# Performance work log

Hardware: AMD Instinct MI355X
Metric: run time of the kernel (lower is better)

The kernel has to match this reference:

```python
import jax, jax.numpy as jnp
import numpy as np
from jax import lax

B, T, HID, H, DK, DV, K = 2, 2048, 1024, 16, 64, 64, 4
SCALE = float(DK) ** -0.5
EPS = 1e-5


def setup_inputs() -> dict:
    key = jax.random.key(0)
    ks = jax.random.split(key, 12)
    n = lambda k, sh, s=0.02: (jax.random.normal(k, sh, jnp.float32) * s)
    return {
        "x": jax.random.normal(ks[0], (B, T, HID), jnp.float32),
        "Wq": n(ks[1], (H * DK, HID)),
        "Wk": n(ks[2], (H * DK, HID)),
        "Wv": n(ks[3], (H * DV, HID)),
        "Wa": n(ks[4], (H * DV, HID)), "ba": jnp.zeros((H * DV,), jnp.float32),
        "Wb": n(ks[5], (H, HID)), "bb": jnp.zeros((H,), jnp.float32),
        "Wg": n(ks[6], (H * DV, HID)),
        "Wo": n(ks[7], (HID, H * DV)),
        "qcw": n(ks[8], (H * DK, 1, K), 0.3), "qcb": jnp.zeros((H * DK,), jnp.float32),
        "kcw": n(ks[9], (H * DK, 1, K), 0.3), "kcb": jnp.zeros((H * DK,), jnp.float32),
        "vcw": n(ks[10], (H * DV, 1, K), 0.3), "vcb": jnp.zeros((H * DV,), jnp.float32),
        "ln_w": jnp.ones((DV,), jnp.float32), "ln_b": jnp.zeros((DV,), jnp.float32),
    }


def _causal_dwconv_silu(z, w, b):
    # z: [B,T,C], w: [C,1,K] depthwise. Conv1d(padding=K-1) then slice[:T] == causal left-pad.
    zc = z.transpose(0, 2, 1)  # [B,C,T]
    y = lax.conv_general_dilated(zc, w, (1,), [(K - 1, 0)],
                                 dimension_numbers=("NCH", "OIH", "NCH"),
                                 feature_group_count=zc.shape[1])
    return jax.nn.silu((y + b[None, :, None]).transpose(0, 2, 1))


def reference(x, Wq, Wk, Wv, Wa, ba, Wb, bb, Wg, Wo,
              qcw, qcb, kcw, kcb, vcw, vcb, ln_w, ln_b):
    Bb, Tt, _ = x.shape
    q = _causal_dwconv_silu(x @ Wq.T, qcw, qcb).reshape(Bb, Tt, H, DK)
    k = _causal_dwconv_silu(x @ Wk.T, kcw, kcb).reshape(Bb, Tt, H, DK) * SCALE
    v = _causal_dwconv_silu(x @ Wv.T, vcw, vcb).reshape(Bb, Tt, H, DV)
    a = jax.nn.sigmoid(x @ Wa.T + ba).reshape(Bb, Tt, H, DV)
    beta = jax.nn.sigmoid(x @ Wb.T + bb)  # [B,T,H]

    def step(S, inp):
        qt, kt, vt, at, bt = inp  # qt/kt: [B,H,DK], vt/at: [B,H,DV], bt: [B,H]
        err = jnp.einsum("bhij,bhj->bhi", S, kt) - vt          # S@k - v
        S = at[..., None] * S - bt[..., None, None] * (err[..., None] * kt[:, :, None, :])
        o = jnp.einsum("bhij,bhj->bhi", S, qt)                 # S@q
        return S, o

    xs = tuple(jnp.moveaxis(t, 1, 0) for t in (q, k, v, a, beta))  # time-leading
    S0 = jnp.zeros((Bb, H, DV, DK), x.dtype)
    _, o = lax.scan(step, S0, xs)
    o = jnp.moveaxis(o, 0, 1)  # [B,T,H,DV]

    mu = o.mean(-1, keepdims=True)
    var = ((o - mu) ** 2).mean(-1, keepdims=True)
    o = (o - mu) / jnp.sqrt(var + EPS) * ln_w + ln_b

    g = jax.nn.sigmoid(x @ Wg.T).reshape(Bb, Tt, H, DV)
    o = (o * g).reshape(Bb, Tt, H * DV)
    return o @ Wo.T
```

## Files before the change

kernel.cpp:

```cpp
#include <hip/hip_runtime.h>
#include <hip/hip_bf16.h>
#include <cstdint>


using bf16 = __hip_bfloat16;
typedef __bf16 bf16x8 __attribute__((ext_vector_type(8)));
typedef __bf16 bf16x4v __attribute__((ext_vector_type(4)));
typedef float f32x4 __attribute__((ext_vector_type(4)));
typedef float f32x2 __attribute__((ext_vector_type(2)));
typedef unsigned int u32x4 __attribute__((ext_vector_type(4)));
typedef unsigned int u32x2 __attribute__((ext_vector_type(2)));

__device__ __forceinline__ __bf16 cvt_bf16(float f) {
  __hip_bfloat16 h = (__hip_bfloat16)f;
  return *reinterpret_cast<__bf16*>(&h);
}
__device__ __forceinline__ void async_copy16(const void* g, void* l) {
  __builtin_amdgcn_global_load_lds((const __attribute__((address_space(1))) void*)g,
                                   (__attribute__((address_space(3))) void*)l,
                                   16, 0, 0);
}
__device__ __forceinline__ float bcf(unsigned int u) { return __builtin_bit_cast(float, u); }
template <int CTRL>
__device__ __forceinline__ float dpp_f(float x) {
  int y = __builtin_amdgcn_update_dpp(0, __builtin_bit_cast(int, x), CTRL, 0xF, 0xF, true);
  return __builtin_bit_cast(float, y);
}

__global__ __launch_bounds__(256) void cvt_plane_kernel(
    const float* __restrict__ in, bf16* __restrict__ out)
{
  size_t i = ((size_t)blockIdx.x * 256 + threadIdx.x) * 4;
  float4 f = *(const float4*)(in + i);
  bf16x4v t;
  t[0] = cvt_bf16(f.x); t[1] = cvt_bf16(f.y); t[2] = cvt_bf16(f.z); t[3] = cvt_bf16(f.w);
  *(bf16x4v*)((__bf16*)out + i) = t;
}

template <int MODE, bool A_FP32>
__global__ __launch_bounds__(256) void gemm_bt(
    const void* __restrict__ Av, const float* __restrict__ Bt,
    const float* __restrict__ bias, float* __restrict__ Cf, bf16* __restrict__ Cb,
    int M, int N, int K)
{
  __shared__ __align__(16) __bf16 As[128 * 32];
  __shared__ __align__(16) __bf16 Bs[128 * 32];

  const int tid  = threadIdx.x;
  const int lane = tid & 63;
  const int wave = tid >> 6;
  const int tile_m = blockIdx.y * 128;
  const int tile_n = blockIdx.x * 128;
  const int wm = (wave >> 1) * 64;
  const int wn = (wave & 1) * 64;

  const int srow = lane >> 2;
  const int scol = (lane & 3) * 8;

  f32x4 acc[4][4];
#pragma unroll
  for (int i = 0; i < 4; ++i)
#pragma unroll
    for (int j = 0; j < 4; ++j) acc[i][j] = {0.f, 0.f, 0.f, 0.f};

  for (int k0 = 0; k0 < K; k0 += 32) {
    float4 b0[2], b1[2], a0[2], a1[2];
#pragma unroll
    for (int s = 0; s < 2; ++s) {
      int brow = tile_n + s * 64 + wave * 16 + srow;
      if (brow > N - 1) brow = N - 1;
      const float* bp = Bt + (size_t)brow * K + k0 + scol;
      b0[s] = *(const float4*)bp;
      b1[s] = *(const float4*)(bp + 4);
      if (A_FP32) {
        int arow = tile_m + s * 64 + wave * 16 + srow;
        const float* ap = (const float*)Av + (size_t)arow * K + k0 + scol;
        a0[s] = *(const float4*)ap;
        a1[s] = *(const float4*)(ap + 4);
      }
    }
    __syncthreads();
#pragma unroll
    for (int s = 0; s < 2; ++s) {
      if (!A_FP32) {
        int arow = tile_m + s * 64 + wave * 16 + srow;
        async_copy16((const __bf16*)Av + (size_t)arow * K + k0 + scol,
                     &As[(s * 64 + wave * 16 + srow) * 32 + scol]);
      } else {
        bf16x8 ua;
        ua[0] = cvt_bf16(a0[s].x); ua[1] = cvt_bf16(a0[s].y);
        ua[2] = cvt_bf16(a0[s].z); ua[3] = cvt_bf16(a0[s].w);
        ua[4] = cvt_bf16(a1[s].x); ua[5] = cvt_bf16(a1[s].y);
        ua[6] = cvt_bf16(a1[s].z); ua[7] = cvt_bf16(a1[s].w);
        *(bf16x8*)&As[(s * 64 + wave * 16 + srow) * 32 + scol] = ua;
      }
      bf16x8 u;
      u[0] = cvt_bf16(b0[s].x); u[1] = cvt_bf16(b0[s].y);
      u[2] = cvt_bf16(b0[s].z); u[3] = cvt_bf16(b0[s].w);
      u[4] = cvt_bf16(b1[s].x); u[5] = cvt_bf16(b1[s].y);
      u[6] = cvt_bf16(b1[s].z); u[7] = cvt_bf16(b1[s].w);
      *(bf16x8*)&Bs[(s * 64 + wave * 16 + srow) * 32 + scol] = u;
    }
    __syncthreads();

    bf16x8 af[4], bfr[4];
#pragma unroll
    for (int i = 0; i < 4; ++i)
      af[i] = *(const bf16x8*)&As[(wm + i * 16 + (lane & 15)) * 32 + (lane >> 4) * 8];
#pragma unroll
    for (int j = 0; j < 4; ++j)
      bfr[j] = *(const bf16x8*)&Bs[(wn + j * 16 + (lane & 15)) * 32 + (lane >> 4) * 8];

#pragma unroll
    for (int i = 0; i < 4; ++i)
#pragma unroll
      for (int j = 0; j < 4; ++j)
        acc[i][j] = __builtin_amdgcn_mfma_f32_16x16x32_bf16(af[i], bfr[j], acc[i][j], 0, 0, 0);
  }

#pragma unroll
  for (int i = 0; i < 4; ++i) {
#pragma unroll
    for (int j = 0; j < 4; ++j) {
#pragma unroll
      for (int r = 0; r < 4; ++r) {
        int gm = tile_m + wm + i * 16 + (lane >> 4) * 4 + r;
        int gn = tile_n + wn + j * 16 + (lane & 15);
        if (gn < N) {
          float val = acc[i][j][r];
          if (MODE == 3 || MODE == 5) {
            float bv = bias ? bias[gn] : 0.f;
            val = 1.f / (1.f + __expf(-(val + bv)));
          }
          if (MODE == 4)      Cf[(size_t)gm * N + gn] = val;
          else if (MODE == 5) Cf[(size_t)gn * M + gm] = val;
          else                Cb[(size_t)gm * N + gn] = (bf16)val;
        }
      }
    }
  }
}

__global__ __launch_bounds__(256) void mega_gemm(
    const bf16* __restrict__ Av, const float* __restrict__ Wq,
    const float* __restrict__ Wk, const float* __restrict__ Wv,
    const float* __restrict__ Wa, const float* __restrict__ ba,
    bf16* __restrict__ C4, int M, int K)
{
  __shared__ __align__(16) __bf16 As[128 * 32];
  __shared__ __align__(16) __bf16 Bs[128 * 32];

  const int tid  = threadIdx.x;
  const int lane = tid & 63;
  const int wave = tid >> 6;
  const int tile_m = blockIdx.y * 128;
  const int tile_n = blockIdx.x * 128;
  const int grp = tile_n >> 10;
  const int tnl = tile_n & 1023;
  const float* Bt = (grp == 0) ? Wq : (grp == 1) ? Wk : (grp == 2) ? Wv : Wa;
  const int wm = (wave >> 1) * 64;
  const int wn = (wave & 1) * 64;

  const int srow = lane >> 2;
  const int scol = (lane & 3) * 8;

  f32x4 acc[4][4];
#pragma unroll
  for (int i = 0; i < 4; ++i)
#pragma unroll
    for (int j = 0; j < 4; ++j) acc[i][j] = {0.f, 0.f, 0.f, 0.f};

  for (int k0 = 0; k0 < K; k0 += 32) {
    float4 b0[2], b1[2];
#pragma unroll
    for (int s = 0; s < 2; ++s) {
      int brow = tnl + s * 64 + wave * 16 + srow;
      const float* bp = Bt + (size_t)brow * K + k0 + scol;
      b0[s] = *(const float4*)bp;
      b1[s] = *(const float4*)(bp + 4);
    }
    __syncthreads();
#pragma unroll
    for (int s = 0; s < 2; ++s) {
      int arow = tile_m + s * 64 + wave * 16 + srow;
      async_copy16((const __bf16*)Av + (size_t)arow * K + k0 + scol,
                   &As[(s * 64 + wave * 16 + srow) * 32 + scol]);
      bf16x8 u;
      u[0] = cvt_bf16(b0[s].x); u[1] = cvt_bf16(b0[s].y);
      u[2] = cvt_bf16(b0[s].z); u[3] = cvt_bf16(b0[s].w);
      u[4] = cvt_bf16(b1[s].x); u[5] = cvt_bf16(b1[s].y);
      u[6] = cvt_bf16(b1[s].z); u[7] = cvt_bf16(b1[s].w);
      *(bf16x8*)&Bs[(s * 64 + wave * 16 + srow) * 32 + scol] = u;
    }
    __syncthreads();

    bf16x8 af[4], bfr[4];
#pragma unroll
    for (int i = 0; i < 4; ++i)
      af[i] = *(const bf16x8*)&As[(wm + i * 16 + (lane & 15)) * 32 + (lane >> 4) * 8];
#pragma unroll
    for (int j = 0; j < 4; ++j)
      bfr[j] = *(const bf16x8*)&Bs[(wn + j * 16 + (lane & 15)) * 32 + (lane >> 4) * 8];

#pragma unroll
    for (int i = 0; i < 4; ++i)
#pragma unroll
      for (int j = 0; j < 4; ++j)
        acc[i][j] = __builtin_amdgcn_mfma_f32_16x16x32_bf16(af[i], bfr[j], acc[i][j], 0, 0, 0);
  }

  bf16* Cp = (bf16*)((__bf16*)C4 + (size_t)grp * M * 1024);
#pragma unroll
  for (int i = 0; i < 4; ++i) {
#pragma unroll
    for (int j = 0; j < 4; ++j) {
#pragma unroll
      for (int r = 0; r < 4; ++r) {
        int gm = tile_m + wm + i * 16 + (lane >> 4) * 4 + r;
        int col = tnl + wn + j * 16 + (lane & 15);
        float val = acc[i][j][r];
        if (grp == 3) val = 1.f / (1.f + __expf(-(val + ba[col])));
        ((__bf16*)Cp)[(size_t)gm * 1024 + col] = cvt_bf16(val);
      }
    }
  }
}

__global__ __launch_bounds__(256) void conv_silu_kernel(
    const bf16* __restrict__ z, const float* __restrict__ w,
    const float* __restrict__ bias, bf16* __restrict__ out, float scale)
{
  int idx = blockIdx.x * 256 + threadIdx.x;
  int c8 = idx & 127;
  int m  = idx >> 7;
  int t  = m & 2047;
  int c0 = c8 * 8;

  const __bf16* base = (const __bf16*)z + (size_t)m * 1024 + c0;
  const bf16x8 zzero = __builtin_bit_cast(bf16x8, (u32x4){0u, 0u, 0u, 0u});
  bf16x8 z3 = *(const bf16x8*)base;
  bf16x8 z2 = (t >= 1) ? *(const bf16x8*)(base - 1024) : zzero;
  bf16x8 z1 = (t >= 2) ? *(const bf16x8*)(base - 2048) : zzero;
  bf16x8 z0 = (t >= 3) ? *(const bf16x8*)(base - 3072) : zzero;

  const float* wp = w + c0 * 4;
  bf16x8 res;
#pragma unroll
  for (int e = 0; e < 8; ++e) {
    float4 we = *(const float4*)(wp + e * 4);
    float acc = bias[c0 + e] + (float)z3[e] * we.w;
    acc += (float)z2[e] * we.z;
    acc += (float)z1[e] * we.y;
    acc += (float)z0[e] * we.x;
    float s = acc / (1.f + __expf(-acc));
    res[e] = cvt_bf16(s * scale);
  }
  *(bf16x8*)((__bf16*)out + (size_t)m * 1024 + c0) = res;
}

__global__ __launch_bounds__(256) void kk_kernel(
    const bf16* __restrict__ k, const float* __restrict__ betab,
    float* __restrict__ G)
{
  int tid = blockIdx.x * 256 + threadIdx.x;
  int out = tid >> 2;
  int j   = tid & 3;
  int h = out >> 12;
  int m = out & 4095;
  int t = m & 2047;
  float s = 0.f;
  if (t > 0) {
    const __bf16* r1 = (const __bf16*)k + (size_t)m * 1024 + h * 64 + j * 16;
    const __bf16* r0 = r1 - 1024;
    bf16x8 a0 = *(const bf16x8*)r0;
    bf16x8 a1 = *(const bf16x8*)(r0 + 8);
    bf16x8 b0 = *(const bf16x8*)r1;
    bf16x8 b1 = *(const bf16x8*)(r1 + 8);
#pragma unroll
    for (int e = 0; e < 8; ++e)
      s += (float)a0[e] * (float)b0[e] + (float)a1[e] * (float)b1[e];
  }
  s += __shfl_xor(s, 1);
  s += __shfl_xor(s, 2);
  if (j == 0) G[out] = betab[out] * s;
}

#define SCAN_STEP(i, KN0, KN1, Q0, Q1, WV, WA, BT, GT, LAST)                  \
  {                                                                           \
    const float vr = ((i) & 1) ? bcf((WV) & 0xffff0000u) : bcf((WV) << 16);   \
    const float ar = ((i) & 1) ? bcf((WA) & 0xffff0000u) : bcf((WA) << 16);   \
    float unxt = 0.f;                                                         \
    f32x2 k2n0 = {0.f, 0.f}, k2n1 = {0.f, 0.f};                               \
    if (!(LAST)) {                                                            \
      k2n0 = unpk(KN0); k2n1 = unpk(KN1);                                     \
      f32x2 dd = S20 * k2n0; dd += S21 * k2n1;                                \
      unxt = dd[0] + dd[1];                                                   \
      unxt += dpp_f<0xB1>(unxt);  unxt += dpp_f<0x4E>(unxt);                  \
      unxt += dpp_f<0x141>(unxt); unxt += dpp_f<0x140>(unxt);                 \
    } else { Sold0 = S20; Sold1 = S21; }                                      \
    float A_ = (BT) * __builtin_fmaf(aprev, u, -vr);                          \
    cc = __builtin_fmaf(-cc, (GT), A_);                                       \
    f32x2 q20 = unpk(Q0), q21 = unpk(Q1);                                     \
    const f32x2 cc2 = {cc, cc}, arv = {ar, ar};                               \
    f32x2 oo;                                                                 \
    { f32x2 t0 = cc2 * k2c0; S20 = arv * S20 - t0; oo = S20 * q20;            \
      f32x2 t1 = cc2 * k2c1; S21 = arv * S21 - t1; oo += S21 * q21; }         \
    so[(i)][lane] = oo[0] + oo[1];                                            \
    aprev = ar;                                                               \
    if (!(LAST)) { k2c0 = k2n0; k2c1 = k2n1; u = unxt; }                      \
  }

#define LOADG(KS, QS, VS, AS, BS, GS, g)                                      \
  KS = *(const u32x4*)&skT[buf][sg][(g) * 8];                                 \
  QS = *(const u32x4*)&sqT[buf][sg][(g) * 8];                                 \
  VS = *(const unsigned int*)&svaT[buf][0][r4][(g) * 2];                      \
  AS = *(const unsigned int*)&svaT[buf][1][r4][(g) * 2];                      \
  BS = *(const f32x2*)&sbeta[c * 16 + (g) * 2];                               \
  GS = *(const f32x2*)&sG[c * 16 + (g) * 2];

__global__ __launch_bounds__(256) void scan_gemm_kernel(
    const bf16* __restrict__ q, const bf16* __restrict__ k,
    const bf16* __restrict__ v, const bf16* __restrict__ a,
    const float* __restrict__ betab, const float* __restrict__ gkk,
    bf16* __restrict__ o,
    const float* __restrict__ x, const float* __restrict__ Wg,
    bf16* __restrict__ gout)
{
  __shared__ __align__(16) __bf16 skT[2][16][72];
  __shared__ __align__(16) __bf16 sqT[2][16][72];
  __shared__ __align__(16) __bf16 svaT[2][2][4][16];
  __shared__ __align__(16) float  so[16][68];
  __shared__ __align__(16) __bf16 so2[16][4];
  __shared__ float sbeta[2048];
  __shared__ float sG[2048];
  __shared__ __align__(16) __bf16 As[128 * 32];
  __shared__ __align__(16) __bf16 Bs[128 * 32];

  if (blockIdx.x >= 512) {
    const int gb   = blockIdx.x - 512;
    const int tid  = threadIdx.x;
    const int lane = tid & 63;
    const int wave = tid >> 6;
    const int tile_m = (gb >> 3) * 128;
    const int tile_n = (gb & 7) * 128;
    const int wm = (wave >> 1) * 64;
    const int wn = (wave & 1) * 64;
    const int srow = lane >> 2;
    const int scol = (lane & 3) * 8;

    f32x4 acc[4][4];
#pragma unroll
    for (int i = 0; i < 4; ++i)
#pragma unroll
      for (int j = 0; j < 4; ++j) acc[i][j] = {0.f, 0.f, 0.f, 0.f};

    for (int k0 = 0; k0 < 1024; k0 += 32) {
      float4 b0[2], b1[2], a0[2], a1[2];
#pragma unroll
      for (int s = 0; s < 2; ++s) {
        int brow = tile_n + s * 64 + wave * 16 + srow;
        const float* bp = Wg + (size_t)brow * 1024 + k0 + scol;
        b0[s] = *(const float4*)bp;
        b1[s] = *(const float4*)(bp + 4);
        int arow = tile_m + s * 64 + wave * 16 + srow;
        const float* ap = x + (size_t)arow * 1024 + k0 + scol;
        a0[s] = *(const float4*)ap;
        a1[s] = *(const float4*)(ap + 4);
      }
      __syncthreads();
#pragma unroll
      for (int s = 0; s < 2; ++s) {
        bf16x8 ua;
        ua[0] = cvt_bf16(a0[s].x); ua[1] = cvt_bf16(a0[s].y);
        ua[2] = cvt_bf16(a0[s].z); ua[3] = cvt_bf16(a0[s].w);
        ua[4] = cvt_bf16(a1[s].x); ua[5] = cvt_bf16(a1[s].y);
        ua[6] = cvt_bf16(a1[s].z); ua[7] = cvt_bf16(a1[s].w);
        *(bf16x8*)&As[(s * 64 + wave * 16 + srow) * 32 + scol] = ua;
        bf16x8 ub;
        ub[0] = cvt_bf16(b0[s].x); ub[1] = cvt_bf16(b0[s].y);
        ub[2] = cvt_bf16(b0[s].z); ub[3] = cvt_bf16(b0[s].w);
        ub[4] = cvt_bf16(b1[s].x); ub[5] = cvt_bf16(b1[s].y);
        ub[6] = cvt_bf16(b1[s].z); ub[7] = cvt_bf16(b1[s].w);
        *(bf16x8*)&Bs[(s * 64 + wave * 16 + srow) * 32 + scol] = ub;
      }
      __syncthreads();

      bf16x8 af[4], bfr[4];
#pragma unroll
      for (int i = 0; i < 4; ++i)
        af[i] = *(const bf16x8*)&As[(wm + i * 16 + (lane & 15)) * 32 + (lane >> 4) * 8];
#pragma unroll
      for (int j = 0; j < 4; ++j)
        bfr[j] = *(const bf16x8*)&Bs[(wn + j * 16 + (lane & 15)) * 32 + (lane >> 4) * 8];

#pragma unroll
      for (int i = 0; i < 4; ++i)
#pragma unroll
        for (int j = 0; j < 4; ++j)
          acc[i][j] = __builtin_amdgcn_mfma_f32_16x16x32_bf16(af[i], bfr[j], acc[i][j], 0, 0, 0);
    }

#pragma unroll
    for (int i = 0; i < 4; ++i)
#pragma unroll
      for (int j = 0; j < 4; ++j)
#pragma unroll
        for (int r = 0; r < 4; ++r) {
          int gm = tile_m + wm + i * 16 + (lane >> 4) * 4 + r;
          int gn = tile_n + wn + j * 16 + (lane & 15);
          float val = 1.f / (1.f + __expf(-acc[i][j][r]));
          gout[(size_t)gm * 1024 + gn] = (bf16)val;
        }
    return;
  }

  if (threadIdx.x >= 64) return;

  const int blk = blockIdx.x;
  const int qd = blk >> 5;
  const int bh = blk & 31;
  const int b = bh >> 4, h = bh & 15;
  const int lane = threadIdx.x;
  const int r4 = lane >> 4;
  const int sg = lane & 15;

  {
    const float* bp = betab + (size_t)h * 4096 + b * 2048;
    const float* gp = gkk   + (size_t)h * 4096 + b * 2048;
    for (int t = lane; t < 2048; t += 64) { sbeta[t] = bp[t]; sG[t] = gp[t]; }
  }

  const size_t bkq = (size_t)b * 2048 * 1024 + h * 64;
  const size_t bva = bkq + qd * 4;
  const __bf16* kp = (const __bf16*)k;
  const __bf16* qp = (const __bf16*)q;

  const int g_st = lane >> 3;
  const int g_cg = (lane & 7) * 8;
  const int sgp  = (lane & 7) * 2;
  const int va_vh = (lane >> 4) & 1;
  const int va_st = lane & 15;

  bf16x8 pk0, pk1, pq0, pq1;
  bf16x4v pva;
  auto fetch = [&](int t0) {
    int st0 = t0 + g_st, st1 = t0 + 8 + g_st;
    pk0 = *(const bf16x8*)(kp + bkq + (size_t)st0 * 1024 + g_cg);
    pk1 = *(const bf16x8*)(kp + bkq + (size_t)st1 * 1024 + g_cg);
    pq0 = *(const bf16x8*)(qp + bkq + (size_t)st0 * 1024 + g_cg);
    pq1 = *(const bf16x8*)(qp + bkq + (size_t)st1 * 1024 + g_cg);
    if (lane < 32) {
      const __bf16* src = va_vh ? (const __bf16*)a : (const __bf16*)v;
      pva = *(const bf16x4v*)(src + bva + (size_t)(t0 + va_st) * 1024);
    }
  };
  auto commit = [&](int cb) {
    {
      u32x4 wk = __builtin_bit_cast(u32x4, pk0);
      u32x4 wq = __builtin_bit_cast(u32x4, pq0);
      u32x2 lo, hi;
      lo[0] = wk[0]; lo[1] = wk[1]; hi[0] = wk[2]; hi[1] = wk[3];
      *(u32x2*)&skT[cb][sgp][g_st * 4]     = lo;
      *(u32x2*)&skT[cb][sgp + 1][g_st * 4] = hi;
      lo[0] = wq[0]; lo[1] = wq[1]; hi[0] = wq[2]; hi[1] = wq[3];
      *(u32x2*)&sqT[cb][sgp][g_st * 4]     = lo;
      *(u32x2*)&sqT[cb][sgp + 1][g_st * 4] = hi;
    }
    {
      u32x4 wk = __builtin_bit_cast(u32x4, pk1);
      u32x4 wq = __builtin_bit_cast(u32x4, pq1);
      u32x2 lo, hi;
      lo[0] = wk[0]; lo[1] = wk[1]; hi[0] = wk[2]; hi[1] = wk[3];
      *(u32x2*)&skT[cb][sgp][(8 + g_st) * 4]     = lo;
      *(u32x2*)&skT[cb][sgp + 1][(8 + g_st) * 4] = hi;
      lo[0] = wq[0]; lo[1] = wq[1]; hi[0] = wq[2]; hi[1] = wq[3];
      *(u32x2*)&sqT[cb][sgp][(8 + g_st) * 4]     = lo;
      *(u32x2*)&sqT[cb][sgp + 1][(8 + g_st) * 4] = hi;
    }
    if (lane < 32) {
#pragma unroll
      for (int r = 0; r < 4; ++r) svaT[cb][va_vh][r][va_st] = pva[r];
    }
  };

  fetch(0); commit(0);

  f32x2 S20 = {0.f, 0.f}, S21 = {0.f, 0.f};
  f32x2 Sold0 = {0.f, 0.f}, Sold1 = {0.f, 0.f};
  float u = 0.f, cc = 0.f, aprev = 0.f;

  auto unpk = [&](unsigned int w) -> f32x2 {
    f32x2 r; r[0] = bcf(w << 16); r[1] = bcf(w & 0xffff0000u); return r;
  };

  for (int c = 0; c < 128; ++c) {
    const int buf = c & 1;
    const bool hasNext = (c + 1 < 128);

    if (hasNext) fetch((c + 1) * 16);

    u32x4 kA, qA, kB, qB, kC, qC;
    unsigned int vA, aA, vB, aB, vC, aC;
    f32x2 bA, gA, bB, gB, bC, gC;

    LOADG(kA, qA, vA, aA, bA, gA, 0)
    LOADG(kB, qB, vB, aB, bB, gB, 1)
    LOADG(kC, qC, vC, aC, bC, gC, 2)

    f32x2 k2c0 = unpk(kA[0]);
    f32x2 k2c1 = unpk(kA[1]);
    {
      f32x2 dd = Sold0 * k2c0;
      dd += Sold1 * k2c1;
      float un = dd[0] + dd[1];
      un += dpp_f<0xB1>(un);
      un += dpp_f<0x4E>(un);
      un += dpp_f<0x141>(un);
      un += dpp_f<0x140>(un);
      u = un;
    }

    SCAN_STEP(0,  kA[2], kA[3], qA[0], qA[1], vA, aA, bA[0], gA[0], false)
    SCAN_STEP(1,  kB[0], kB[1], qA[2], qA[3], vA, aA, bA[1], gA[1], false)
    LOADG(kA, qA, vA, aA, bA, gA, 3)
    SCAN_STEP(2,  kB[2], kB[3], qB[0], qB[1], vB, aB, bB[0], gB[0], false)
    SCAN_STEP(3,  kC[0], kC[1], qB[2], qB[3], vB, aB, bB[1], gB[1], false)
    LOADG(kB, qB, vB, aB, bB, gB, 4)
    SCAN_STEP(4,  kC[2], kC[3], qC[0], qC[1], vC, aC, bC[0], gC[0], false)
    SCAN_STEP(5,  kA[0], kA[1], qC[2], qC[3], vC, aC, bC[1], gC[1], false)
    LOADG(kC, qC, vC, aC, bC, gC, 5)
    SCAN_STEP(6,  kA[2], kA[3], qA[0], qA[1], vA, aA, bA[0], gA[0], false)
    SCAN_STEP(7,  kB[0], kB[1], qA[2], qA[3], vA, aA, bA[1], gA[1], false)
    LOADG(kA, qA, vA, aA, bA, gA, 6)
    SCAN_STEP(8,  kB[2], kB[3], qB[0], qB[1], vB, aB, bB[0], gB[0], false)
    SCAN_STEP(9,  kC[0], kC[1], qB[2], qB[3], vB, aB, bB[1], gB[1], false)
    LOADG(kB, qB, vB, aB, bB, gB, 7)
    SCAN_STEP(10, kC[2], kC[3], qC[0], qC[1], vC, aC, bC[0], gC[0], false)
    SCAN_STEP(11, kA[0], kA[1], qC[2], qC[3], vC, aC, bC[1], gC[1], false)
    SCAN_STEP(12, kA[2], kA[3], qA[0], qA[1], vA, aA, bA[0], gA[0], false)
    SCAN_STEP(13, kB[0], kB[1], qA[2], qA[3], vA, aA, bA[1], gA[1], false)
    SCAN_STEP(14, kB[2], kB[3], qB[0], qB[1], vB, aB, bB[0], gB[0], false)
    SCAN_STEP(15, kB[2], kB[3], qB[2], qB[3], vB, aB, bB[1], gB[1], true)

    {
      int st = lane >> 2, rr = lane & 3;
      float4 A0 = *(const float4*)&so[st][rr * 16];
      float4 A1 = *(const float4*)&so[st][rr * 16 + 4];
      float4 A2 = *(const float4*)&so[st][rr * 16 + 8];
      float4 A3 = *(const float4*)&so[st][rr * 16 + 12];
      float s = (((A0.x + A0.y) + (A0.z + A0.w)) + ((A1.x + A1.y) + (A1.z + A1.w)))
              + (((A2.x + A2.y) + (A2.z + A2.w)) + ((A3.x + A3.y) + (A3.z + A3.w)));
      so2[st][rr] = cvt_bf16(s);
    }
    if (lane < 16)
      *(bf16x4v*)((__bf16*)o + bva + (size_t)(c * 16 + lane) * 1024) =
          *(const bf16x4v*)&so2[lane][0];

    if (hasNext) commit(buf ^ 1);
  }
}

__global__ __launch_bounds__(256) void ln_gate_kernel(
    const bf16* __restrict__ o, const bf16* __restrict__ g,
    const float* __restrict__ lnw, const float* __restrict__ lnb,
    bf16* __restrict__ out)
{
  int row = blockIdx.x * 4 + (threadIdx.x >> 6);
  int lane = threadIdx.x & 63;
  size_t idx = (size_t)row * 64 + lane;
  float xv = (float)o[idx];
  float mu = xv;
#pragma unroll
  for (int s = 1; s < 64; s <<= 1) mu += __shfl_xor(mu, s);
  mu *= (1.f / 64.f);
  float d = xv - mu;
  float vv = d * d;
#pragma unroll
  for (int s = 1; s < 64; s <<= 1) vv += __shfl_xor(vv, s);
  vv *= (1.f / 64.f);
  float y = d * rsqrtf(vv + 1e-5f) * lnw[lane] + lnb[lane];
  y *= (float)g[idx];
  out[idx] = (bf16)y;
}

extern "C" void kernel_launch(void* const* d_in, const int* in_sizes, int n_in,
                              void* d_out, int out_size, void* d_ws, size_t ws_size,
                              hipStream_t stream)
{
  const float* x   = (const float*)d_in[0];
  const float* Wq  = (const float*)d_in[1];
  const float* Wk  = (const float*)d_in[2];
  const float* Wv  = (const float*)d_in[3];
  const float* Wa  = (const float*)d_in[4];
  const float* ba  = (const float*)d_in[5];
  const float* Wb  = (const float*)d_in[6];
  const float* bb  = (const float*)d_in[7];
  const float* Wg  = (const float*)d_in[8];
  const float* Wo  = (const float*)d_in[9];
  const float* qcw = (const float*)d_in[10];
  const float* qcb = (const float*)d_in[11];
  const float* kcw = (const float*)d_in[12];
  const float* kcb = (const float*)d_in[13];
  const float* vcw = (const float*)d_in[14];
  const float* vcb = (const float*)d_in[15];
  const float* lnw = (const float*)d_in[16];
  const float* lnb = (const float*)d_in[17];

  const int M = 4096, HID = 1024;
  const size_t PLANE = (size_t)M * HID;
  const size_t PB = PLANE * sizeof(bf16);

  char* ws = (char*)d_ws;
  float* outf  = (float*)d_out;
  float* betab = outf;
  float* gkk   = (float*)((char*)d_out + 256 * 1024);
  bf16*  ob    = (bf16*)((char*)d_out + 8 * 1024 * 1024);

  const bool rich = (ws_size >= 5 * PB + 1024);

  dim3 blk(256);
  dim3 g8(8, 32);
  int nconv = (int)((size_t)M * 128 / 256);

  if (rich) {
    bf16* P0 = (bf16*)(ws);
    bf16* P1 = (bf16*)(ws + PB);
    bf16* P2 = (bf16*)(ws + 2 * PB);
    bf16* P3 = (bf16*)(ws + 3 * PB);
    bf16* P4 = (bf16*)(ws + 4 * PB);
    bf16* xb = (bf16*)d_out;

    cvt_plane_kernel<<<(int)(PLANE / 1024), blk, 0, stream>>>(x, xb);
    mega_gemm<<<dim3(32, 32), blk, 0, stream>>>(xb, Wq, Wk, Wv, Wa, ba, P0, M, HID);
    conv_silu_kernel<<<nconv, blk, 0, stream>>>(P0, qcw, qcb, P4, 1.f);
    conv_silu_kernel<<<nconv, blk, 0, stream>>>(P1, kcw, kcb, P0, 0.125f);
    conv_silu_kernel<<<nconv, blk, 0, stream>>>(P2, vcw, vcb, P1, 1.f);
    gemm_bt<5, false><<<dim3(1, 32), blk, 0, stream>>>(xb, Wb, bb, betab, nullptr, M, 16, HID);
    kk_kernel<<<1024, blk, 0, stream>>>(P0, betab, gkk);
    scan_gemm_kernel<<<768, blk, 0, stream>>>(P4, P0, P1, P3, betab, gkk, ob,
                                              x, Wg, P2);
    ln_gate_kernel<<<M * 16 / 4, blk, 0, stream>>>(ob, P2, lnw, lnb, P3);
    gemm_bt<4, false><<<g8, blk, 0, stream>>>(P3, Wo, nullptr, outf, nullptr, M, HID, HID);
  } else {
    bf16* P  = (bf16*)(ws);
    bf16* qb = (bf16*)(ws + PB);
    bf16* kb = (bf16*)(ws + 2 * PB);
    bf16* vb = (bf16*)(ws + 3 * PB);

    gemm_bt<2, true><<<g8, blk, 0, stream>>>(x, Wq, nullptr, nullptr, P, M, HID, HID);
    conv_silu_kernel<<<nconv, blk, 0, stream>>>(P, qcw, qcb, qb, 1.f);
    gemm_bt<2, true><<<g8, blk, 0, stream>>>(x, Wk, nullptr, nullptr, P, M, HID, HID);
    conv_silu_kernel<<<nconv, blk, 0, stream>>>(P, kcw, kcb, kb, 0.125f);
    gemm_bt<2, true><<<g8, blk, 0, stream>>>(x, Wv, nullptr, nullptr, P, M, HID, HID);
    conv_silu_kernel<<<nconv, blk, 0, stream>>>(P, vcw, vcb, vb, 1.f);
    gemm_bt<3, true><<<g8, blk, 0, stream>>>(x, Wa, ba, nullptr, P, M, HID, HID);
    gemm_bt<5, true><<<dim3(1, 32), blk, 0, stream>>>(x, Wb, bb, betab, nullptr, M, 16, HID);
    kk_kernel<<<1024, blk, 0, stream>>>(kb, betab, gkk);
    scan_gemm_kernel<<<512, blk, 0, stream>>>(qb, kb, vb, P, betab, gkk, ob,
                                              x, Wg, nullptr);
    gemm_bt<3, true><<<g8, blk, 0, stream>>>(x, Wg, nullptr, nullptr, qb, M, HID, HID);
    ln_gate_kernel<<<M * 16 / 4, blk, 0, stream>>>(ob, qb, lnw, lnb, kb);
    gemm_bt<4, false><<<g8, blk, 0, stream>>>(kb, Wo, nullptr, outf, nullptr, M, HID, HID);
  }
}
```

Baseline: 510.6 us.

## Pre-convert projection weights to bf16 and fold beta GEMM into mega GEMM

The weights Wq/Wk/Wv/Wa are converted to bf16 once in an extended conversion kernel alongside x. The mega GEMM can then load B tiles with async global-to-LDS copies, the same way it loads A, instead of converting fp32 in registers on every k-step. The small beta projection becomes an extra column of blocks in the mega GEMM, which removes a separate launch. Buffers are reassigned across the output region and workspace to hold the bf16 weights. The cost is an extra conversion pass over 16 MB of weights per call and some branchy, mostly idle work in the beta blocks.

```diff
diff --git a/kernel.cpp b/kernel.cpp
--- a/kernel.cpp
+++ b/kernel.cpp
@@ -27,14 +27,29 @@
   return __builtin_bit_cast(float, y);
 }
 
-__global__ __launch_bounds__(256) void cvt_plane_kernel(
-    const float* __restrict__ in, bf16* __restrict__ out)
+__global__ __launch_bounds__(256) void cvtw_kernel(
+    const float* __restrict__ x, const float* __restrict__ Wq,
+    const float* __restrict__ Wk, const float* __restrict__ Wv,
+    const float* __restrict__ Wa, bf16* __restrict__ xb, bf16* __restrict__ w4b)
 {
-  size_t i = ((size_t)blockIdx.x * 256 + threadIdx.x) * 4;
-  float4 f = *(const float4*)(in + i);
+  int blk = blockIdx.x;
+  const float* src;
+  __bf16* dst;
+  size_t off;
+  if (blk < 4096) {
+    src = x; dst = (__bf16*)xb;
+    off = (size_t)blk * 1024 + threadIdx.x * 4;
+  } else {
+    int wb = blk - 4096;
+    int wi = wb >> 10;
+    src = (wi == 0) ? Wq : (wi == 1) ? Wk : (wi == 2) ? Wv : Wa;
+    dst = (__bf16*)w4b + (size_t)wi * 1024 * 1024;
+    off = (size_t)(wb & 1023) * 1024 + threadIdx.x * 4;
+  }
+  float4 f = *(const float4*)(src + off);
   bf16x4v t;
   t[0] = cvt_bf16(f.x); t[1] = cvt_bf16(f.y); t[2] = cvt_bf16(f.z); t[3] = cvt_bf16(f.w);
-  *(bf16x4v*)((__bf16*)out + i) = t;
+  *(bf16x4v*)(dst + off) = t;
 }
 
 template <int MODE, bool A_FP32>
@@ -141,11 +156,11 @@
   }
 }
 
-__global__ __launch_bounds__(256) void mega_gemm(
-    const bf16* __restrict__ Av, const float* __restrict__ Wq,
-    const float* __restrict__ Wk, const float* __restrict__ Wv,
-    const float* __restrict__ Wa, const float* __restrict__ ba,
-    bf16* __restrict__ C4, int M, int K)
+__global__ __launch_bounds__(256) void mega_gemm2(
+    const bf16* __restrict__ Av, const bf16* __restrict__ W4b,
+    const float* __restrict__ Wb, const float* __restrict__ bb,
+    const float* __restrict__ ba, bf16* __restrict__ C4,
+    float* __restrict__ betab)
 {
   __shared__ __align__(16) __bf16 As[128 * 32];
   __shared__ __align__(16) __bf16 Bs[128 * 32];
@@ -154,10 +169,10 @@
   const int lane = tid & 63;
   const int wave = tid >> 6;
   const int tile_m = blockIdx.y * 128;
-  const int tile_n = blockIdx.x * 128;
+  const bool isbeta = (blockIdx.x >= 32);
+  const int tile_n = isbeta ? 0 : blockIdx.x * 128;
   const int grp = tile_n >> 10;
   const int tnl = tile_n & 1023;
-  const float* Bt = (grp == 0) ? Wq : (grp == 1) ? Wk : (grp == 2) ? Wv : Wa;
   const int wm = (wave >> 1) * 64;
   const int wn = (wave & 1) * 64;
 
@@ -170,27 +185,38 @@
 #pragma unroll
     for (int j = 0; j < 4; ++j) acc[i][j] = {0.f, 0.f, 0.f, 0.f};
 
-  for (int k0 = 0; k0 < K; k0 += 32) {
+  const __bf16* Wp = (const __bf16*)W4b + (size_t)grp * 1024 * 1024;
+
+  for (int k0 = 0; k0 < 1024; k0 += 32) {
     float4 b0[2], b1[2];
-#pragma unroll
-    for (int s = 0; s < 2; ++s) {
-      int brow = tnl + s * 64 + wave * 16 + srow;
-      const float* bp = Bt + (size_t)brow * K + k0 + scol;
-      b0[s] = *(const float4*)bp;
-      b1[s] = *(const float4*)(bp + 4);
+    if (isbeta) {
+#pragma unroll
+      for (int s = 0; s < 2; ++s) {
+        int brow = s * 64 + wave * 16 + srow;
+        if (brow > 15) brow = 15;
+        const float* bp = Wb + (size_t)brow * 1024 + k0 + scol;
+        b0[s] = *(const float4*)bp;
+        b1[s] = *(const float4*)(bp + 4);
+      }
     }
     __syncthreads();
 #pragma unroll
     for (int s = 0; s < 2; ++s) {
       int arow = tile_m + s * 64 + wave * 16 + srow;
-      async_copy16((const __bf16*)Av + (size_t)arow * K + k0 + scol,
+      async_copy16((const __bf16*)Av + (size_t)arow * 1024 + k0 + scol,
                    &As[(s * 64 + wave * 16 + srow) * 32 + scol]);
-      bf16x8 u;
-      u[0] = cvt_bf16(b0[s].x); u[1] = cvt_bf16(b0[s].y);
-      u[2] = cvt_bf16(b0[s].z); u[3] = cvt_bf16(b0[s].w);
-      u[4] = cvt_bf16(b1[s].x); u[5] = cvt_bf16(b1[s].y);
-      u[6] = cvt_bf16(b1[s].z); u[7] = cvt_bf16(b1[s].w);
-      *(bf16x8*)&Bs[(s * 64 + wave * 16 + srow) * 32 + scol] = u;
+      if (!isbeta) {
+        int brow = tnl + s * 64 + wave * 16 + srow;
+        async_copy16(Wp + (size_t)brow * 1024 + k0 + scol,
+                     &Bs[(s * 64 + wave * 16 + srow) * 32 + scol]);
+      } else {
+        bf16x8 u;
+        u[0] = cvt_bf16(b0[s].x); u[1] = cvt_bf16(b0[s].y);
+        u[2] = cvt_bf16(b0[s].z); u[3] = cvt_bf16(b0[s].w);
+        u[4] = cvt_bf16(b1[s].x); u[5] = cvt_bf16(b1[s].y);
+        u[6] = cvt_bf16(b1[s].z); u[7] = cvt_bf16(b1[s].w);
+        *(bf16x8*)&Bs[(s * 64 + wave * 16 + srow) * 32 + scol] = u;
+      }
     }
     __syncthreads();
 
@@ -209,20 +235,34 @@
         acc[i][j] = __builtin_amdgcn_mfma_f32_16x16x32_bf16(af[i], bfr[j], acc[i][j], 0, 0, 0);
   }
 
-  bf16* Cp = (bf16*)((__bf16*)C4 + (size_t)grp * M * 1024);
-#pragma unroll
-  for (int i = 0; i < 4; ++i) {
-#pragma unroll
-    for (int j = 0; j < 4; ++j) {
-#pragma unroll
-      for (int r = 0; r < 4; ++r) {
-        int gm = tile_m + wm + i * 16 + (lane >> 4) * 4 + r;
-        int col = tnl + wn + j * 16 + (lane & 15);
-        float val = acc[i][j][r];
-        if (grp == 3) val = 1.f / (1.f + __expf(-(val + ba[col])));
-        ((__bf16*)Cp)[(size_t)gm * 1024 + col] = cvt_bf16(val);
-      }
-    }
+  if (!isbeta) {
+    bf16* Cp = (bf16*)((__bf16*)C4 + (size_t)grp * 4096 * 1024);
+#pragma unroll
+    for (int i = 0; i < 4; ++i)
+#pragma unroll
+      for (int j = 0; j < 4; ++j)
+#pragma unroll
+        for (int r = 0; r < 4; ++r) {
+          int gm = tile_m + wm + i * 16 + (lane >> 4) * 4 + r;
+          int col = tnl + wn + j * 16 + (lane & 15);
+          float val = acc[i][j][r];
+          if (grp == 3) val = 1.f / (1.f + __expf(-(val + ba[col])));
+          ((__bf16*)Cp)[(size_t)gm * 1024 + col] = cvt_bf16(val);
+        }
+  } else {
+#pragma unroll
+    for (int i = 0; i < 4; ++i)
+#pragma unroll
+      for (int j = 0; j < 4; ++j)
+#pragma unroll
+        for (int r = 0; r < 4; ++r) {
+          int gm = tile_m + wm + i * 16 + (lane >> 4) * 4 + r;
+          int gn = wn + j * 16 + (lane & 15);
+          if (gn < 16) {
+            float val = 1.f / (1.f + __expf(-(acc[i][j][r] + bb[gn])));
+            betab[(size_t)gn * 4096 + gm] = val;
+          }
+        }
   }
 }
 
@@ -611,11 +651,7 @@
   const size_t PB = PLANE * sizeof(bf16);
 
   char* ws = (char*)d_ws;
-  float* outf  = (float*)d_out;
-  float* betab = outf;
-  float* gkk   = (float*)((char*)d_out + 256 * 1024);
-  bf16*  ob    = (bf16*)((char*)d_out + 8 * 1024 * 1024);
-
+  float* outf = (float*)d_out;
   const bool rich = (ws_size >= 5 * PB + 1024);
 
   dim3 blk(256);
@@ -628,24 +664,31 @@
     bf16* P2 = (bf16*)(ws + 2 * PB);
     bf16* P3 = (bf16*)(ws + 3 * PB);
     bf16* P4 = (bf16*)(ws + 4 * PB);
-    bf16* xb = (bf16*)d_out;
-
-    cvt_plane_kernel<<<(int)(PLANE / 1024), blk, 0, stream>>>(x, xb);
-    mega_gemm<<<dim3(32, 32), blk, 0, stream>>>(xb, Wq, Wk, Wv, Wa, ba, P0, M, HID);
-    conv_silu_kernel<<<nconv, blk, 0, stream>>>(P0, qcw, qcb, P4, 1.f);
-    conv_silu_kernel<<<nconv, blk, 0, stream>>>(P1, kcw, kcb, P0, 0.125f);
+    bf16*  xb    = (bf16*)d_out;
+    bf16*  W4b   = (bf16*)((char*)d_out + 8 * 1024 * 1024);
+    bf16*  Kb    = xb;
+    bf16*  Qb    = W4b;
+    float* betab = (float*)P4;
+    float* gkk   = (float*)((char*)P4 + 256 * 1024);
+
+    cvtw_kernel<<<8192, blk, 0, stream>>>(x, Wq, Wk, Wv, Wa, xb, W4b);
+    mega_gemm2<<<dim3(33, 32), blk, 0, stream>>>(xb, W4b, Wb, bb, ba, P0, betab);
+    conv_silu_kernel<<<nconv, blk, 0, stream>>>(P0, qcw, qcb, Qb, 1.f);
+    conv_silu_kernel<<<nconv, blk, 0, stream>>>(P1, kcw, kcb, Kb, 0.125f);
     conv_silu_kernel<<<nconv, blk, 0, stream>>>(P2, vcw, vcb, P1, 1.f);
-    gemm_bt<5, false><<<dim3(1, 32), blk, 0, stream>>>(xb, Wb, bb, betab, nullptr, M, 16, HID);
-    kk_kernel<<<1024, blk, 0, stream>>>(P0, betab, gkk);
-    scan_gemm_kernel<<<768, blk, 0, stream>>>(P4, P0, P1, P3, betab, gkk, ob,
+    kk_kernel<<<1024, blk, 0, stream>>>(Kb, betab, gkk);
+    scan_gemm_kernel<<<768, blk, 0, stream>>>(Qb, Kb, P1, P3, betab, gkk, P0,
                                               x, Wg, P2);
-    ln_gate_kernel<<<M * 16 / 4, blk, 0, stream>>>(ob, P2, lnw, lnb, P3);
-    gemm_bt<4, false><<<g8, blk, 0, stream>>>(P3, Wo, nullptr, outf, nullptr, M, HID, HID);
+    ln_gate_kernel<<<M * 16 / 4, blk, 0, stream>>>(P0, P2, lnw, lnb, P1);
+    gemm_bt<4, false><<<g8, blk, 0, stream>>>(P1, Wo, nullptr, outf, nullptr, M, HID, HID);
   } else {
     bf16* P  = (bf16*)(ws);
     bf16* qb = (bf16*)(ws + PB);
     bf16* kb = (bf16*)(ws + 2 * PB);
     bf16* vb = (bf16*)(ws + 3 * PB);
+    float* betab = (float*)d_out;
+    float* gkk   = (float*)((char*)d_out + 256 * 1024);
+    bf16*  ob    = (bf16*)((char*)d_out + 8 * 1024 * 1024);
 
     gemm_bt<2, true><<<g8, blk, 0, stream>>>(x, Wq, nullptr, nullptr, P, M, HID, HID);
     conv_silu_kernel<<<nconv, blk, 0, stream>>>(P, qcw, qcb, qb, 1.f);
```

Result: faster. 469.7 us (-8.0%).
